# Optimization experiments

Measured on AMD Instinct MI355X. Metric: run time of the kernel, lower is better.

## Reference

```python
import jax, jax.numpy as jnp
import numpy as np

N_NODES, E_TOT, E_ACT = 20000, 250000, 200000
LAT, OH = 128, 128
M0, M1, M2 = 64, 32, 16            # irreps_out: 64x0e + 32x1o + 16x2e
D_IR = M0 + 3 * M1 + 5 * M2        # 240
G = M1 + M2                        # gate scalars (48)
T0 = M0 + G                        # tp m=0 scalar channels (112)
I0, I1, I2 = 3 * M0, 3 * M1, 3 * M2  # tp input muls (center|edge|neighbor)


def _split(x, m0, m1, m2):
    e = x.shape[0]
    return (x[:, :m0],
            x[:, m0:m0 + 3 * m1].reshape(e, m1, 3),
            x[:, m0 + 3 * m1:].reshape(e, m2, 5))


def _merge(s0, s1, s2):
    e = s0.shape[0]
    return jnp.concatenate([s0, s1.reshape(e, -1), s2.reshape(e, -1)], axis=-1)


def _mlp(x, ws, bs):
    for i, (w, b) in enumerate(zip(ws, bs)):
        x = x @ w + b
        if i < len(ws) - 1:
            x = jax.nn.silu(x)
    return x


def _forward(latents, node_features, edge_features, cutoff_coeffs, edge_one_hot,
             wigner_D1, wigner_D2,
             W0, W1r, W1i, W2r, W2i, Gw, Gb,
             P0, P0b, P1, P2, Ew, Eb, ln_g, ln_b,
             A1, A1b, A2, A2b, A3, A3b,
             B1, B1b, B2, B2b, B3, B3b,
             O0, O1, O2,
             edge_index, active_edges):
    ec = edge_index[0][active_edges]
    en = edge_index[1][active_edges]
    # gather node features per edge (equivariant_norm_type='none' -> identity norms)
    nc0, nc1, nc2 = _split(node_features[ec], M0, M1, M2)
    ef0, ef1, ef2 = _split(edge_features, M0, M1, M2)
    nn0, nn1, nn2 = _split(node_features[en], M0, M1, M2)
    x0 = jnp.concatenate([nc0, ef0, nn0], -1)   # [E,192]
    x1 = jnp.concatenate([nc1, ef1, nn1], 1)    # [E,96,3]
    x2 = jnp.concatenate([nc2, ef2, nn2], 1)    # [E,48,5]
    lat_a = latents[active_edges]
    # --- SO(2) linear: rotate into edge frame, per-m mixing, latent gains, rotate back ---
    r1 = jnp.einsum('eij,euj->eui', wigner_D1, x1)
    r2 = jnp.einsum('eij,euj->eui', wigner_D2, x2)
    in0 = jnp.concatenate([x0, r1[:, :, 1], r2[:, :, 2]], -1)   # m=0 [E,336]
    o_m0 = in0 @ W0.T                                           # [E,160]
    ip1 = jnp.concatenate([r1[:, :, 2], r2[:, :, 3]], -1)       # m=+1 [E,144]
    im1 = jnp.concatenate([r1[:, :, 0], r2[:, :, 1]], -1)       # m=-1
    op1 = ip1 @ W1r.T - im1 @ W1i.T                             # [E,48]
    on1 = ip1 @ W1i.T + im1 @ W1r.T
    op2 = r2[:, :, 4] @ W2r.T - r2[:, :, 0] @ W2i.T             # [E,16]
    on2 = r2[:, :, 4] @ W2i.T + r2[:, :, 0] @ W2r.T
    g = lat_a @ Gw + Gb                                         # per-edge gains [E,224]
    o_m0 = o_m0 * g[:, :160]
    g1 = g[:, 160:208]; g2 = g[:, 208:224]
    op1 = op1 * g1; on1 = on1 * g1; op2 = op2 * g2; on2 = on2 * g2
    y0 = o_m0[:, :T0]
    y1 = jnp.stack([on1[:, :M1], o_m0[:, T0:T0 + M1], op1[:, :M1]], -1)          # [E,32,3]
    y2 = jnp.stack([on2, on1[:, M1:], o_m0[:, T0 + M1:], op1[:, M1:], op2], -1)  # [E,16,5]
    y1 = jnp.einsum('eji,euj->eui', wigner_D1, y1)
    y2 = jnp.einsum('eji,euj->eui', wigner_D2, y2)
    # --- gate activation ---
    gates = jax.nn.sigmoid(y0[:, M0:])
    z0 = jax.nn.silu(y0[:, :M0])
    z1 = y1 * gates[:, :M1, None]
    z2 = y2 * gates[:, M1:, None]
    # --- lin_post: per-l channel mixing, fan-in normalized, bias on scalars ---
    z0 = z0 @ P0.T / np.sqrt(M0) + P0b
    z1 = jnp.einsum('uv,evm->eum', P1, z1) / np.sqrt(M1)
    z2 = jnp.einsum('uv,evm->eum', P2, z2) / np.sqrt(M2)
    scalars = z0                                               # taken before weighting
    # --- E3ElementLinear: per-edge per-channel weights from latents ---
    w = lat_a @ Ew + Eb                                        # [E,112]
    z0 = z0 * w[:, :M0]
    z1 = z1 * w[:, M0:M0 + M1, None]
    z2 = z2 * w[:, M0 + M1:, None]
    new_edge = _merge(z0, z1, z2)
    # --- latent update: LN -> mlp1(ln_lat||scalars) -> mlp2(h||one_hot) -> cutoff ---
    mu = lat_a.mean(-1, keepdims=True)
    var = ((lat_a - mu) ** 2).mean(-1, keepdims=True)
    ln_lat = (lat_a - mu) * jax.lax.rsqrt(var + 1e-5) * ln_g + ln_b
    h = _mlp(jnp.concatenate([ln_lat, scalars], -1), (A1, A2, A3), (A1b, A2b, A3b))
    h = _mlp(jnp.concatenate([h, edge_one_hot], -1), (B1, B2, B3), (B1b, B2b, B3b))
    new_lat = cutoff_coeffs[active_edges][:, None] * h
    # --- residual update (res_update_params buffer = 0) ---
    u = jax.nn.sigmoid(jnp.asarray(0.0, new_edge.dtype))
    c_old = jax.lax.rsqrt(u * u + 1.0)
    c_new = u * c_old
    edge_out = c_old * edge_features + c_new * new_edge        # identity residual path
    latents_out = latents.at[active_edges].set(c_new * new_lat + c_old * lat_a)
    # --- layer one-hot tensor product (uvu with 128x0e) ---
    f0, f1, f2 = _split(edge_out, M0, M1, M2)
    s = 1.0 / np.sqrt(OH)
    t0 = f0 * (edge_one_hot @ O0.T) * s
    t1 = f1 * (edge_one_hot @ O1.T)[:, :, None] * s
    t2 = f2 * (edge_one_hot @ O2.T)[:, :, None] * s
    edge_out = edge_out + _merge(t0, t1, t2)
    return edge_out, latents_out


def setup_inputs() -> dict:
    key = jax.random.key(0)
    ks = iter(jax.random.split(key, 64))
    nrm = lambda sh, s=0.05: jax.random.normal(next(ks), sh, jnp.float32) * s
    inp = dict(
        latents=nrm((E_TOT, LAT), 1.0),
        node_features=nrm((N_NODES, D_IR), 1.0),
        edge_features=nrm((E_ACT, D_IR), 1.0),
        cutoff_coeffs=jax.random.uniform(next(ks), (E_TOT,), jnp.float32),
        edge_one_hot=jax.random.uniform(next(ks), (E_ACT, OH), jnp.float32),
        wigner_D1=nrm((E_ACT, 3, 3), 0.5),
        wigner_D2=nrm((E_ACT, 5, 5), 0.3),
        W0=nrm((160, I0 + I1 + I2)), W1r=nrm((48, 144)), W1i=nrm((48, 144)),
        W2r=nrm((16, 48)), W2i=nrm((16, 48)),
        Gw=nrm((LAT, 224)), Gb=jnp.ones((224,), jnp.float32),
        P0=nrm((M0, M0)), P0b=nrm((M0,)), P1=nrm((M1, M1)), P2=nrm((M2, M2)),
        Ew=nrm((LAT, M0 + M1 + M2)), Eb=jnp.ones((M0 + M1 + M2,), jnp.float32),
        ln_g=jnp.ones((LAT,), jnp.float32), ln_b=jnp.zeros((LAT,), jnp.float32),
        A1=nrm((LAT + M0, LAT)), A1b=nrm((LAT,)),
        A2=nrm((LAT, LAT)), A2b=nrm((LAT,)),
        A3=nrm((LAT, LAT)), A3b=nrm((LAT,)),
        B1=nrm((LAT + OH, LAT)), B1b=nrm((LAT,)),
        B2=nrm((LAT, LAT)), B2b=nrm((LAT,)),
        B3=nrm((LAT, LAT)), B3b=nrm((LAT,)),
        O0=nrm((M0, OH)), O1=nrm((M1, OH)), O2=nrm((M2, OH)),
        edge_index=jax.random.randint(next(ks), (2, E_TOT), 0, N_NODES, jnp.int32),
        active_edges=jnp.sort(jax.random.permutation(next(ks), E_TOT)[:E_ACT]).astype(jnp.int32),
    )
    return inp


def reference(latents, node_features, edge_features, cutoff_coeffs, edge_one_hot,
              wigner_D1, wigner_D2,
              W0, W1r, W1i, W2r, W2i, Gw, Gb,
              P0, P0b, P1, P2, Ew, Eb, ln_g, ln_b,
              A1, A1b, A2, A2b, A3, A3b,
              B1, B1b, B2, B2b, B3, B3b,
              O0, O1, O2, edge_index, active_edges):
    return _forward(latents, node_features, edge_features, cutoff_coeffs, edge_one_hot,
                    wigner_D1, wigner_D2,
                    W0, W1r, W1i, W2r, W2i, Gw, Gb,
                    P0, P0b, P1, P2, Ew, Eb, ln_g, ln_b,
                    A1, A1b, A2, A2b, A3, A3b,
                    B1, B1b, B2, B2b, B3, B3b,
                    O0, O1, O2, edge_index, active_edges)
```

## Files before the change

### kernel.cpp

```cpp
#include <hip/hip_runtime.h>

typedef unsigned short us_t;
typedef short bf16x8 __attribute__((ext_vector_type(8)));
typedef float f32x4 __attribute__((ext_vector_type(4)));

#define E_ACT 200000
#define E_TOT 250000
#define DIR   240
#define C_OLD 0.8944271909999159f
#define C_NEW 0.4472135954999579f
#define S_OH  0.08838834764831845f

#define WO_W0   0
#define WO_W1P  56320
#define WO_W1M  70144
#define WO_W2P  83968
#define WO_W2M  85504
#define WO_GW   87040
#define WO_EW   115712
#define WO_A1   130048
#define WO_A2   154624
#define WO_A3   171008
#define WO_B1   187392
#define WO_B2   220160
#define WO_B3   236544
#define WO_O0   252928
#define WO_O1   261120
#define WO_O2   265216
#define WO_P0T  267264
#define WO_P1T  271360
#define WO_P2T  272384
#define W_TOTAL 272896

__device__ __forceinline__ float b2f(us_t u) { return __uint_as_float(((unsigned)u) << 16); }
__device__ __forceinline__ us_t f2b(float f) {
    unsigned x = __float_as_uint(f);
    return (us_t)((x + 0x7fffu + ((x >> 16) & 1u)) >> 16);
}
__device__ __forceinline__ float sigm(float x) { return 1.0f / (1.0f + __expf(-x)); }

#define MFMA(a,b,c) __builtin_amdgcn_mfma_f32_16x16x32_bf16((a),(b),(c),0,0,0)

__global__ __launch_bounds__(256) void prep_kernel(
    const float* __restrict__ W0, const float* __restrict__ W1r, const float* __restrict__ W1i,
    const float* __restrict__ W2r, const float* __restrict__ W2i,
    const float* __restrict__ Gw, const float* __restrict__ Ew,
    const float* __restrict__ A1, const float* __restrict__ A2, const float* __restrict__ A3,
    const float* __restrict__ B1, const float* __restrict__ B2, const float* __restrict__ B3,
    const float* __restrict__ O0, const float* __restrict__ O1, const float* __restrict__ O2,
    const float* __restrict__ P0w, const float* __restrict__ P1w, const float* __restrict__ P2w,
    us_t* __restrict__ wb)
{
    int idx = blockIdx.x * 256 + threadIdx.x;
    if (idx >= W_TOTAL) return;
    float v;
    if (idx < WO_W1P) {
        int r = idx, n = r / 352, k = r % 352;
        v = (k < 336) ? W0[n * 336 + k] : 0.f;
    } else if (idx < WO_W1M) {
        int r = idx - WO_W1P, n = r / 288, k = r % 288;
        v = (k < 144) ? W1r[n * 144 + k] : -W1i[n * 144 + (k - 144)];
    } else if (idx < WO_W2P) {
        int r = idx - WO_W1M, n = r / 288, k = r % 288;
        v = (k < 144) ? W1i[n * 144 + k] : W1r[n * 144 + (k - 144)];
    } else if (idx < WO_W2M) {
        int r = idx - WO_W2P, n = r / 96, k = r % 96;
        v = (k < 48) ? W2r[n * 48 + k] : -W2i[n * 48 + (k - 48)];
    } else if (idx < WO_GW) {
        int r = idx - WO_W2M, n = r / 96, k = r % 96;
        v = (k < 48) ? W2i[n * 48 + k] : W2r[n * 48 + (k - 48)];
    } else if (idx < WO_EW) {
        int r = idx - WO_GW, n = r / 128, k = r % 128;
        v = Gw[k * 224 + n];
    } else if (idx < WO_A1) {
        int r = idx - WO_EW, n = r / 128, k = r % 128;
        v = Ew[k * 112 + n];
    } else if (idx < WO_A2) {
        int r = idx - WO_A1, n = r / 192, k = r % 192;
        v = A1[k * 128 + n];
    } else if (idx < WO_A3) {
        int r = idx - WO_A2, n = r / 128, k = r % 128;
        v = A2[k * 128 + n];
    } else if (idx < WO_B1) {
        int r = idx - WO_A3, n = r / 128, k = r % 128;
        v = A3[k * 128 + n];
    } else if (idx < WO_B2) {
        int r = idx - WO_B1, n = r / 256, k = r % 256;
        v = B1[k * 128 + n];
    } else if (idx < WO_B3) {
        int r = idx - WO_B2, n = r / 128, k = r % 128;
        v = B2[k * 128 + n];
    } else if (idx < WO_O0) {
        int r = idx - WO_B3, n = r / 128, k = r % 128;
        v = B3[k * 128 + n];
    } else if (idx < WO_O1) {
        v = O0[idx - WO_O0];
    } else if (idx < WO_O2) {
        v = O1[idx - WO_O1];
    } else if (idx < WO_P0T) {
        v = O2[idx - WO_O2];
    } else if (idx < WO_P1T) {
        v = P0w[idx - WO_P0T];
    } else if (idx < WO_P2T) {
        v = P1w[idx - WO_P1T];
    } else {
        int r = idx - WO_P2T, n = r / 32, k = r % 32;
        v = (k < 16) ? P2w[n * 16 + k] : 0.f;
    }
    wb[idx] = f2b(v);
}

__device__ __forceinline__ void lat_fetch_a(const float* __restrict__ latents,
                                            const int* __restrict__ aes_l,
                                            int lane, bf16x8 a[4])
{
    const int r = lane & 15, g = lane >> 4;
    const float* lp = latents + (size_t)aes_l[r] * 128 + g * 8;
    #pragma unroll
    for (int ks = 0; ks < 4; ++ks) {
        float4 v0 = *(const float4*)(lp + ks * 32);
        float4 v1 = *(const float4*)(lp + ks * 32 + 4);
        bf16x8 av;
        av[0] = (short)f2b(v0.x); av[1] = (short)f2b(v0.y);
        av[2] = (short)f2b(v0.z); av[3] = (short)f2b(v0.w);
        av[4] = (short)f2b(v1.x); av[5] = (short)f2b(v1.y);
        av[6] = (short)f2b(v1.z); av[7] = (short)f2b(v1.w);
        a[ks] = av;
    }
}

__device__ __forceinline__ void gemmW0g(
    const us_t* __restrict__ in0s, const us_t* __restrict__ wbase,
    const bf16x8 latA[4], const float* __restrict__ Gb,
    int nt0, int nt1, us_t* __restrict__ om0g, int lane)
{
    const int r = lane & 15, g = lane >> 4;
    f32x4 w0a = {0.f,0.f,0.f,0.f}, w0b = w0a, ga = w0a, gb2 = w0a;
    const us_t* ap  = in0s + r * 360 + g * 8;
    const us_t* wp0 = wbase + WO_W0 + (size_t)(nt0 * 16 + r) * 352 + g * 8;
    const us_t* wp1 = wbase + WO_W0 + (size_t)(nt1 * 16 + r) * 352 + g * 8;
    #pragma unroll
    for (int ks = 0; ks < 11; ++ks) {
        bf16x8 a = *(const bf16x8*)(ap + ks * 32);
        w0a = MFMA(a, *(const bf16x8*)(wp0 + ks * 32), w0a);
        w0b = MFMA(a, *(const bf16x8*)(wp1 + ks * 32), w0b);
    }
    const us_t* gp0 = wbase + WO_GW + (size_t)(nt0 * 16 + r) * 128 + g * 8;
    const us_t* gp1 = wbase + WO_GW + (size_t)(nt1 * 16 + r) * 128 + g * 8;
    #pragma unroll
    for (int ks = 0; ks < 4; ++ks) {
        ga  = MFMA(latA[ks], *(const bf16x8*)(gp0 + ks * 32), ga);
        gb2 = MFMA(latA[ks], *(const bf16x8*)(gp1 + ks * 32), gb2);
    }
    float b0 = Gb[nt0 * 16 + r], b1 = Gb[nt1 * 16 + r];
    #pragma unroll
    for (int i = 0; i < 4; ++i) {
        int e = g * 4 + i;
        om0g[e * 162 + nt0 * 16 + r] = f2b(w0a[i] * (ga[i] + b0));
        om0g[e * 162 + nt1 * 16 + r] = f2b(w0b[i] * (gb2[i] + b1));
    }
}

__device__ __forceinline__ void gemmW1g(
    const us_t* __restrict__ cact1, const us_t* __restrict__ wbase,
    const bf16x8 latA[4], const float* __restrict__ Gb,
    int j, us_t* __restrict__ cp1g, us_t* __restrict__ cn1g, int lane)
{
    const int r = lane & 15, g = lane >> 4;
    f32x4 p = {0.f,0.f,0.f,0.f}, m = p, gg = p;
    const us_t* ap  = cact1 + r * 296 + g * 8;
    const us_t* wpP = wbase + WO_W1P + (size_t)(j * 16 + r) * 288 + g * 8;
    const us_t* wpM = wbase + WO_W1M + (size_t)(j * 16 + r) * 288 + g * 8;
    #pragma unroll
    for (int ks = 0; ks < 9; ++ks) {
        bf16x8 a = *(const bf16x8*)(ap + ks * 32);
        p = MFMA(a, *(const bf16x8*)(wpP + ks * 32), p);
        m = MFMA(a, *(const bf16x8*)(wpM + ks * 32), m);
    }
    const us_t* gp = wbase + WO_GW + (size_t)(160 + j * 16 + r) * 128 + g * 8;
    #pragma unroll
    for (int ks = 0; ks < 4; ++ks)
        gg = MFMA(latA[ks], *(const bf16x8*)(gp + ks * 32), gg);
    float gb = Gb[160 + j * 16 + r];
    #pragma unroll
    for (int i = 0; i < 4; ++i) {
        int e = g * 4 + i;
        float gv = gg[i] + gb;
        cp1g[e * 50 + j * 16 + r] = f2b(p[i] * gv);
        cn1g[e * 50 + j * 16 + r] = f2b(m[i] * gv);
    }
}

__device__ __forceinline__ void gemmW2g(
    const us_t* __restrict__ cact2, const us_t* __restrict__ wbase,
    const bf16x8 latA[4], const float* __restrict__ Gb,
    us_t* __restrict__ cp2g, us_t* __restrict__ cn2g, int lane)
{
    const int r = lane & 15, g = lane >> 4;
    f32x4 p = {0.f,0.f,0.f,0.f}, m = p, gg = p;
    const us_t* ap  = cact2 + r * 104 + g * 8;
    const us_t* wpP = wbase + WO_W2P + (size_t)r * 96 + g * 8;
    const us_t* wpM = wbase + WO_W2M + (size_t)r * 96 + g * 8;
    #pragma unroll
    for (int ks = 0; ks < 3; ++ks) {
        bf16x8 a = *(const bf16x8*)(ap + ks * 32);
        p = MFMA(a, *(const bf16x8*)(wpP + ks * 32), p);
        m = MFMA(a, *(const bf16x8*)(wpM + ks * 32), m);
    }
    const us_t* gp = wbase + WO_GW + (size_t)(208 + r) * 128 + g * 8;
    #pragma unroll
    for (int ks = 0; ks < 4; ++ks)
        gg = MFMA(latA[ks], *(const bf16x8*)(gp + ks * 32), gg);
    float gb = Gb[208 + r];
    #pragma unroll
    for (int i = 0; i < 4; ++i) {
        int e = g * 4 + i;
        float gv = gg[i] + gb;
        cp2g[e * 18 + r] = f2b(p[i] * gv);
        cn2g[e * 18 + r] = f2b(m[i] * gv);
    }
}

__device__ __forceinline__ void lat_gemm2(const bf16x8 a[4],
    const us_t* __restrict__ wgt, const float* __restrict__ bias,
    int nt0, int nt1, us_t* __restrict__ out, int os, int lane)
{
    const int r = lane & 15, g = lane >> 4;
    f32x4 acc0 = {0.f,0.f,0.f,0.f}, acc1 = {0.f,0.f,0.f,0.f};
    const us_t* wp0 = wgt + (size_t)(nt0 * 16 + r) * 128 + g * 8;
    const us_t* wp1 = wgt + (size_t)(nt1 * 16 + r) * 128 + g * 8;
    #pragma unroll
    for (int ks = 0; ks < 4; ++ks) {
        acc0 = MFMA(a[ks], *(const bf16x8*)(wp0 + ks * 32), acc0);
        acc1 = MFMA(a[ks], *(const bf16x8*)(wp1 + ks * 32), acc1);
    }
    float bi0 = bias[nt0 * 16 + r], bi1 = bias[nt1 * 16 + r];
    #pragma unroll
    for (int i = 0; i < 4; ++i) {
        int e = g * 4 + i;
        out[e * os + nt0 * 16 + r] = f2b(acc0[i] + bi0);
        out[e * os + nt1 * 16 + r] = f2b(acc1[i] + bi1);
    }
}

__device__ __forceinline__ void lat_gemm1(const bf16x8 a[4],
    const us_t* __restrict__ wgt, const float* __restrict__ bias,
    int nt, us_t* __restrict__ out, int os, int lane)
{
    const int r = lane & 15, g = lane >> 4;
    f32x4 acc = {0.f,0.f,0.f,0.f};
    const us_t* wp = wgt + (size_t)(nt * 16 + r) * 128 + g * 8;
    #pragma unroll
    for (int ks = 0; ks < 4; ++ks)
        acc = MFMA(a[ks], *(const bf16x8*)(wp + ks * 32), acc);
    float bi = bias[nt * 16 + r];
    #pragma unroll
    for (int i = 0; i < 4; ++i) {
        int e = g * 4 + i;
        out[e * os + nt * 16 + r] = f2b(acc[i] + bi);
    }
}

template<int KS>
__device__ __forceinline__ f32x4 pgemm(const us_t* __restrict__ actbase, int as,
                                       const us_t* __restrict__ wgt, int kp, int lane)
{
    const int r = lane & 15, g = lane >> 4;
    f32x4 acc = {0.f,0.f,0.f,0.f};
    const us_t* ap = actbase + r * as + g * 8;
    const us_t* wp = wgt + (size_t)r * kp + g * 8;
    #pragma unroll
    for (int ks = 0; ks < KS; ++ks) {
        bf16x8 a = *(const bf16x8*)(ap + ks * 32);
        bf16x8 b = *(const bf16x8*)(wp + ks * 32);
        acc = MFMA(a, b, acc);
    }
    return acc;
}

__global__ __launch_bounds__(256, 3) void k1_kernel(
    const float* __restrict__ latents,
    const float* __restrict__ node_features,
    const float* __restrict__ edge_features,
    const float* __restrict__ wD1,
    const float* __restrict__ wD2,
    const float* __restrict__ Gb,  const float* __restrict__ Eb,
    const float* __restrict__ P0b,
    const int* __restrict__ edge_index, const int* __restrict__ active_edges,
    const us_t* __restrict__ wbase,
    us_t* __restrict__ ne_ws, us_t* __restrict__ scal_ws)
{
    __shared__ __align__(16) char smem[40320];
    us_t* in0s  = (us_t*)(smem);
    us_t* cact1 = (us_t*)(smem + 11520);
    us_t* cact2 = (us_t*)(smem + 20992);
    float* D1l  = (float*)(smem + 24320);
    float* D2l  = (float*)(smem + 25088);
    int*   aes  = (int*)(smem + 26880);
    us_t* om0g  = (us_t*)(smem + 26944);
    us_t* cp1g  = (us_t*)(smem + 32128);
    us_t* cn1g  = (us_t*)(smem + 33728);
    us_t* cp2g  = (us_t*)(smem + 35328);
    us_t* cn2g  = (us_t*)(smem + 35904);
    us_t* wl    = (us_t*)(smem + 36480);
    us_t* z0l   = (us_t*)(smem);
    us_t* z1l   = (us_t*)(smem + 2304);
    us_t* z2l   = (us_t*)(smem + 5632);

    const int t  = threadIdx.x;
    const int e0 = blockIdx.x * 16;

    {
        const int e = t >> 4, l = t & 15;
        const int eg = e0 + e;
        const int ae = active_edges[eg];
        const int ec = edge_index[ae];
        const int en = edge_index[E_TOT + ae];
        if (l == 0) aes[e] = ae;

        float v1  = (l < 9) ? wD1[(size_t)eg * 9 + l] : 0.f;
        float v2a = wD2[(size_t)eg * 25 + l];
        float v2b = (l < 9) ? wD2[(size_t)eg * 25 + 16 + l] : 0.f;
        if (l < 9) D1l[e * 12 + l] = v1;
        D2l[e * 28 + l] = v2a;
        if (l < 9) D2l[e * 28 + 16 + l] = v2b;

        float d1[9], d2[25];
        #pragma unroll
        for (int i = 0; i < 9; ++i)  d1[i] = __shfl(v1, i, 16);
        #pragma unroll
        for (int i = 0; i < 16; ++i) d2[i] = __shfl(v2a, i, 16);
        #pragma unroll
        for (int i = 0; i < 9; ++i)  d2[16 + i] = __shfl(v2b, i, 16);

        const float* pc = node_features + (size_t)ec * DIR;
        const float* pe = edge_features + (size_t)eg * DIR;
        const float* pn = node_features + (size_t)en * DIR;
        us_t* in0 = in0s + e * 360;
        us_t* c1  = cact1 + e * 296;
        us_t* c2  = cact2 + e * 104;

        #pragma unroll
        for (int j = 0; j < 4; ++j) {
            int i = l + 16 * j;
            in0[i]       = f2b(pc[i]);
            in0[64 + i]  = f2b(pe[i]);
            in0[128 + i] = f2b(pn[i]);
        }
        in0[336 + l] = 0;

        #pragma unroll
        for (int jj = 0; jj < 6; ++jj) {
            int u = l + 16 * jj;
            int uu = u & 31;
            const float* sp = (u < 32 ? pc : (u < 64 ? pe : pn)) + 64 + uu * 3;
            float x0 = sp[0], x1 = sp[1], x2 = sp[2];
            float r0 = d1[0] * x0 + d1[1] * x1 + d1[2] * x2;
            float r1 = d1[3] * x0 + d1[4] * x1 + d1[5] * x2;
            float r2 = d1[6] * x0 + d1[7] * x1 + d1[8] * x2;
            c1[144 + u]  = f2b(r0);
            in0[192 + u] = f2b(r1);
            c1[u]        = f2b(r2);
        }
        #pragma unroll
        for (int jj = 0; jj < 3; ++jj) {
            int u = l + 16 * jj;
            int uu = u & 15;
            const float* sp = (u < 16 ? pc : (u < 32 ? pe : pn)) + 160 + uu * 5;
            float x0 = sp[0], x1 = sp[1], x2 = sp[2], x3 = sp[3], x4 = sp[4];
            float r[5];
            #pragma unroll
            for (int i = 0; i < 5; ++i)
                r[i] = d2[i * 5 + 0] * x0 + d2[i * 5 + 1] * x1 + d2[i * 5 + 2] * x2
                     + d2[i * 5 + 3] * x3 + d2[i * 5 + 4] * x4;
            c2[48 + u]   = f2b(r[0]);
            c1[240 + u]  = f2b(r[1]);
            in0[288 + u] = f2b(r[2]);
            c1[96 + u]   = f2b(r[3]);
            c2[u]        = f2b(r[4]);
        }
    }
    __syncthreads();

    {
        const int lane = t & 63, w = t >> 6;
        bf16x8 a[4];
        lat_fetch_a(latents, aes, lane, a);
        if (w == 0) {
            gemmW0g(in0s, wbase, a, Gb, 0, 1, om0g, lane);
            gemmW0g(in0s, wbase, a, Gb, 2, 3, om0g, lane);
        } else if (w == 1) {
            gemmW0g(in0s, wbase, a, Gb, 4, 5, om0g, lane);
            gemmW0g(in0s, wbase, a, Gb, 6, 7, om0g, lane);
        } else if (w == 2) {
            gemmW1g(cact1, wbase, a, Gb, 0, cp1g, cn1g, lane);
            gemmW1g(cact1, wbase, a, Gb, 1, cp1g, cn1g, lane);
            gemmW1g(cact1, wbase, a, Gb, 2, cp1g, cn1g, lane);
        } else {
            gemmW0g(in0s, wbase, a, Gb, 8, 9, om0g, lane);
            gemmW2g(cact2, wbase, a, Gb, cp2g, cn2g, lane);
            lat_gemm2(a, wbase + WO_EW, Eb, 0, 1, wl, 120, lane);
            lat_gemm2(a, wbase + WO_EW, Eb, 2, 3, wl, 120, lane);
            lat_gemm2(a, wbase + WO_EW, Eb, 4, 5, wl, 120, lane);
            lat_gemm1(a, wbase + WO_EW, Eb, 6, wl, 120, lane);
        }
    }
    __syncthreads();

    {
        const int e = t >> 4, l = t & 15;
        const float* D1e = D1l + e * 12;
        const float* D2e = D2l + e * 28;
        #pragma unroll
        for (int uu = 0; uu < 2; ++uu) {
            int u = l + uu * 16;
            float j0 = b2f(cn1g[e * 50 + u]);
            float j1 = b2f(om0g[e * 162 + 112 + u]);
            float j2 = b2f(cp1g[e * 50 + u]);
            float gate = sigm(b2f(om0g[e * 162 + 64 + u]));
            #pragma unroll
            for (int i = 0; i < 3; ++i) {
                float yr = D1e[0 * 3 + i] * j0 + D1e[1 * 3 + i] * j1 + D1e[2 * 3 + i] * j2;
                z1l[e * 104 + i * 32 + u] = f2b(yr * gate);
            }
        }
        {
            int u = l;
            float j0 = b2f(cn2g[e * 18 + u]);
            float j1 = b2f(cn1g[e * 50 + 32 + u]);
            float j2 = b2f(om0g[e * 162 + 144 + u]);
            float j3 = b2f(cp1g[e * 50 + 32 + u]);
            float j4 = b2f(cp2g[e * 18 + u]);
            float gate = sigm(b2f(om0g[e * 162 + 96 + u]));
            #pragma unroll
            for (int i = 0; i < 5; ++i) {
                float yr = D2e[0 * 5 + i] * j0 + D2e[1 * 5 + i] * j1 + D2e[2 * 5 + i] * j2
                         + D2e[3 * 5 + i] * j3 + D2e[4 * 5 + i] * j4;
                z2l[e * 168 + i * 32 + u] = f2b(yr * gate);
                z2l[e * 168 + i * 32 + 16 + u] = 0;
            }
        }
        #pragma unroll
        for (int ii = 0; ii < 4; ++ii) {
            int c = l + 16 * ii;
            float v = b2f(om0g[e * 162 + c]);
            z0l[e * 72 + c] = f2b(v * sigm(v));
        }
    }
    __syncthreads();

    {
        const int lane = t & 63, w = t >> 6;
        const int r = lane & 15, g = lane >> 4;
        if (w < 2) {
            #pragma unroll
            for (int jj = 0; jj < 2; ++jj) {
                int nt = 2 * w + jj;
                f32x4 acc = pgemm<2>(z0l, 72, wbase + WO_P0T + nt * 16 * 64, 64, lane);
                int n = nt * 16 + r;
                float bi = P0b[n];
                #pragma unroll
                for (int i = 0; i < 4; ++i) {
                    int e = g * 4 + i, eg = e0 + e;
                    float z0p = acc[i] * 0.125f + bi;
                    scal_ws[(size_t)eg * 64 + n] = f2b(z0p);
                    ne_ws[(size_t)eg * 240 + n] = f2b(z0p * b2f(wl[e * 120 + n]));
                }
            }
        } else if (w == 2) {
            #pragma unroll
            for (int m = 0; m < 3; ++m) {
                #pragma unroll
                for (int nt = 0; nt < 2; ++nt) {
                    f32x4 acc = pgemm<1>(z1l + m * 32, 104,
                                         wbase + WO_P1T + nt * 16 * 32, 32, lane);
                    int u = nt * 16 + r;
                    #pragma unroll
                    for (int i = 0; i < 4; ++i) {
                        int e = g * 4 + i, eg = e0 + e;
                        float wv = b2f(wl[e * 120 + 64 + u]);
                        ne_ws[(size_t)eg * 240 + 64 + u * 3 + m] =
                            f2b(acc[i] * 0.17677669529663687f * wv);
                    }
                }
            }
        } else if (w == 3) {
            #pragma unroll
            for (int m = 0; m < 5; ++m) {
                f32x4 acc = pgemm<1>(z2l + m * 32, 168, wbase + WO_P2T, 32, lane);
                int u = r;
                #pragma unroll
                for (int i = 0; i < 4; ++i) {
                    int e = g * 4 + i, eg = e0 + e;
                    float wv = b2f(wl[e * 120 + 96 + u]);
                    ne_ws[(size_t)eg * 240 + 160 + u * 5 + m] =
                        f2b(acc[i] * 0.25f * wv);
                }
            }
        }
    }
}

template<int KS, bool SILU>
__device__ __forceinline__ void mlayer(
    const us_t* __restrict__ actA, const us_t* __restrict__ actB, int split, int as,
    const us_t* __restrict__ wgt, int kp, const float* __restrict__ bias,
    us_t* __restrict__ out, int os, int lane, int w)
{
    const int r = lane & 15, g = lane >> 4;
    const int n0 = 2 * w * 16, n1 = n0 + 16;
    f32x4 a00 = {0.f,0.f,0.f,0.f}, a01 = a00, a10 = a00, a11 = a00;
    const us_t* wp0 = wgt + (size_t)(n0 + r) * kp + g * 8;
    const us_t* wp1 = wgt + (size_t)(n1 + r) * kp + g * 8;
    #pragma unroll
    for (int ks = 0; ks < KS; ++ks) {
        const us_t* ab = (ks < split) ? (actA + ks * 32) : (actB + (ks - split) * 32);
        bf16x8 f0 = *(const bf16x8*)(ab + r * as + g * 8);
        bf16x8 f1 = *(const bf16x8*)(ab + (16 + r) * as + g * 8);
        bf16x8 b0 = *(const bf16x8*)(wp0 + ks * 32);
        bf16x8 b1 = *(const bf16x8*)(wp1 + ks * 32);
        a00 = MFMA(f0, b0, a00); a01 = MFMA(f0, b1, a01);
        a10 = MFMA(f1, b0, a10); a11 = MFMA(f1, b1, a11);
    }
    float bi0 = bias[n0 + r], bi1 = bias[n1 + r];
    #pragma unroll
    for (int i = 0; i < 4; ++i) {
        int eA = g * 4 + i, eB = 16 + g * 4 + i;
        float v;
        v = a00[i] + bi0; if (SILU) v *= sigm(v); out[eA * os + n0 + r] = f2b(v);
        v = a01[i] + bi1; if (SILU) v *= sigm(v); out[eA * os + n1 + r] = f2b(v);
        v = a10[i] + bi0; if (SILU) v *= sigm(v); out[eB * os + n0 + r] = f2b(v);
        v = a11[i] + bi1; if (SILU) v *= sigm(v); out[eB * os + n1 + r] = f2b(v);
    }
}

__global__ __launch_bounds__(256) void k2_kernel(
    const float* __restrict__ latents, const float* __restrict__ cutoff,
    const float* __restrict__ one_hot,
    const float* __restrict__ ln_g, const float* __restrict__ ln_b,
    const float* __restrict__ A1b, const float* __restrict__ A2b, const float* __restrict__ A3b,
    const float* __restrict__ B1b, const float* __restrict__ B2b, const float* __restrict__ B3b,
    const int* __restrict__ active_edges,
    const us_t* __restrict__ wbase,
    const us_t* __restrict__ scal_ws, us_t* __restrict__ ohw_ws,
    float* __restrict__ out_lat)
{
    __shared__ __align__(16) char smem[39424];
    us_t* x_lds = (us_t*)(smem);
    us_t* h_a   = (us_t*)(smem + 12800);
    us_t* h_b   = (us_t*)(smem + 21504);
    us_t* ohl   = (us_t*)(smem + 30208);
    int*  aes_l = (int*)(smem + 38912);
    float* cut_l= (float*)(smem + 39040);

    const int t  = threadIdx.x;
    const int e0 = blockIdx.x * 32;
    const int lane = t & 63, w = t >> 6;

    {
        int ee = t >> 3, l8 = t & 7;
        int ae = active_edges[e0 + ee];
        if (l8 == 0) { aes_l[ee] = ae; cut_l[ee] = cutoff[ae]; }
        const float* lp = latents + (size_t)ae * 128 + l8 * 16;
        float xs[16];
        #pragma unroll
        for (int q = 0; q < 4; ++q) {
            float4 v = *(const float4*)(lp + q * 4);
            xs[q * 4 + 0] = v.x; xs[q * 4 + 1] = v.y;
            xs[q * 4 + 2] = v.z; xs[q * 4 + 3] = v.w;
        }
        float s1 = 0.f, s2 = 0.f;
        #pragma unroll
        for (int i = 0; i < 16; ++i) { s1 += xs[i]; s2 += xs[i] * xs[i]; }
        #pragma unroll
        for (int off = 1; off < 8; off <<= 1) {
            s1 += __shfl_xor(s1, off, 8);
            s2 += __shfl_xor(s2, off, 8);
        }
        float mu  = s1 * (1.f / 128.f);
        float var = s2 * (1.f / 128.f) - mu * mu;
        float rstd = rsqrtf(var + 1e-5f);
        #pragma unroll
        for (int i = 0; i < 16; ++i) {
            int li = l8 * 16 + i;
            x_lds[ee * 200 + li] = f2b((xs[i] - mu) * rstd * ln_g[li] + ln_b[li]);
        }
    }
    for (int idx = t; idx < 32 * 16; idx += 256) {
        int ee = idx >> 4, j = idx & 15;
        *(ushort4*)&x_lds[ee * 200 + 128 + j * 4] =
            *(const ushort4*)&scal_ws[(size_t)(e0 + ee) * 64 + j * 4];
    }
    for (int idx = t; idx < 32 * 32; idx += 256) {
        int ee = idx >> 5, j = idx & 31;
        float4 ov = *(const float4*)&one_hot[(size_t)(e0 + ee) * 128 + j * 4];
        ushort4 s; s.x = f2b(ov.x); s.y = f2b(ov.y); s.z = f2b(ov.z); s.w = f2b(ov.w);
        *(ushort4*)&ohl[ee * 136 + j * 4] = s;
    }
    __syncthreads();

    mlayer<6, true>(x_lds, x_lds, 6, 200, wbase + WO_A1, 192, A1b, h_a, 136, lane, w);
    __syncthreads();
    mlayer<4, true>(h_a, h_a, 4, 136, wbase + WO_A2, 128, A2b, h_b, 136, lane, w);
    __syncthreads();
    mlayer<4, false>(h_b, h_b, 4, 136, wbase + WO_A3, 128, A3b, h_a, 136, lane, w);
    __syncthreads();
    mlayer<8, true>(h_a, ohl, 4, 136, wbase + WO_B1, 256, B1b, h_b, 136, lane, w);
    __syncthreads();
    mlayer<4, true>(h_b, h_b, 4, 136, wbase + WO_B2, 128, B2b, h_a, 136, lane, w);
    __syncthreads();
    {
        const int r = lane & 15, g = lane >> 4;
        const int n0 = 2 * w * 16, n1 = n0 + 16;
        f32x4 a00 = {0.f,0.f,0.f,0.f}, a01 = a00, a10 = a00, a11 = a00;
        const us_t* wp0 = wbase + WO_B3 + (size_t)(n0 + r) * 128 + g * 8;
        const us_t* wp1 = wbase + WO_B3 + (size_t)(n1 + r) * 128 + g * 8;
        #pragma unroll
        for (int ks = 0; ks < 4; ++ks) {
            bf16x8 f0 = *(const bf16x8*)(h_a + ks * 32 + r * 136 + g * 8);
            bf16x8 f1 = *(const bf16x8*)(h_a + ks * 32 + (16 + r) * 136 + g * 8);
            bf16x8 b0 = *(const bf16x8*)(wp0 + ks * 32);
            bf16x8 b1 = *(const bf16x8*)(wp1 + ks * 32);
            a00 = MFMA(f0, b0, a00); a01 = MFMA(f0, b1, a01);
            a10 = MFMA(f1, b0, a10); a11 = MFMA(f1, b1, a11);
        }
        float bi0 = B3b[n0 + r], bi1 = B3b[n1 + r];
        #pragma unroll
        for (int i = 0; i < 4; ++i) {
            int eA = g * 4 + i, eB = 16 + g * 4 + i;
            int aeA = aes_l[eA], aeB = aes_l[eB];
            float cA = C_NEW * cut_l[eA], cB = C_NEW * cut_l[eB];
            float* oA = out_lat + (size_t)aeA * 128;
            float* oB = out_lat + (size_t)aeB * 128;
            const float* lA = latents + (size_t)aeA * 128;
            const float* lB = latents + (size_t)aeB * 128;
            oA[n0 + r] = cA * (a00[i] + bi0) + C_OLD * lA[n0 + r];
            oA[n1 + r] = cA * (a01[i] + bi1) + C_OLD * lA[n1 + r];
            oB[n0 + r] = cB * (a10[i] + bi0) + C_OLD * lB[n0 + r];
            oB[n1 + r] = cB * (a11[i] + bi1) + C_OLD * lB[n1 + r];
        }
    }

    {
        const int r = lane & 15, g = lane >> 4;
        const int cnt = (w == 3) ? 1 : 2;
        #pragma unroll
        for (int ii = 0; ii < 2; ++ii) {
            if (ii >= cnt) break;
            int nt = (ii == 0) ? w : w + 4;
            const us_t* wb2 = (nt < 4) ? (wbase + WO_O0 + (size_t)nt * 16 * 128)
                            : (nt < 6) ? (wbase + WO_O1 + (size_t)(nt - 4) * 16 * 128)
                                       : (wbase + WO_O2);
            f32x4 c0 = {0.f,0.f,0.f,0.f}, c1 = c0;
            const us_t* wp = wb2 + (size_t)r * 128 + g * 8;
            #pragma unroll
            for (int ks = 0; ks < 4; ++ks) {
                bf16x8 f0 = *(const bf16x8*)(ohl + ks * 32 + r * 136 + g * 8);
                bf16x8 f1 = *(const bf16x8*)(ohl + ks * 32 + (16 + r) * 136 + g * 8);
                bf16x8 b = *(const bf16x8*)(wp + ks * 32);
                c0 = MFMA(f0, b, c0); c1 = MFMA(f1, b, c1);
            }
            int n = nt * 16 + r;
            #pragma unroll
            for (int i = 0; i < 4; ++i) {
                int eA = e0 + g * 4 + i, eB = e0 + 16 + g * 4 + i;
                ohw_ws[(size_t)eA * 112 + n] = f2b(c0[i]);
                ohw_ws[(size_t)eB * 112 + n] = f2b(c1[i]);
            }
        }
    }
}

__global__ __launch_bounds__(256) void kfin_kernel(
    const float* __restrict__ edge_features, const us_t* __restrict__ ne_ws,
    const us_t* __restrict__ ohw_ws, float* __restrict__ out_edge)
{
    int idx = blockIdx.x * 256 + threadIdx.x;
    if (idx >= E_ACT * 60) return;
    int e = idx / 60;
    int c0 = (idx - e * 60) * 4;
    float4 ef = *(const float4*)&edge_features[(size_t)e * 240 + c0];
    ushort4 nv = *(const ushort4*)&ne_ws[(size_t)e * 240 + c0];
    float nef[4] = {b2f(nv.x), b2f(nv.y), b2f(nv.z), b2f(nv.w)};
    float eff[4] = {ef.x, ef.y, ef.z, ef.w};
    float4 ov;
    float* op = &ov.x;
    #pragma unroll
    for (int j = 0; j < 4; ++j) {
        int c = c0 + j;
        int o;
        if (c < 64)       o = c;
        else if (c < 160) o = 64 + (c - 64) / 3;
        else              o = 96 + (c - 160) / 5;
        float ohv = b2f(ohw_ws[(size_t)e * 112 + o]);
        op[j] = (C_OLD * eff[j] + C_NEW * nef[j]) * (1.f + S_OH * ohv);
    }
    *(float4*)&out_edge[(size_t)e * 240 + c0] = ov;
}

extern "C" void kernel_launch(void* const* d_in, const int* in_sizes, int n_in,
                              void* d_out, int out_size, void* d_ws, size_t ws_size,
                              hipStream_t stream)
{
    const float* latents  = (const float*)d_in[0];
    const float* node_f   = (const float*)d_in[1];
    const float* edge_f   = (const float*)d_in[2];
    const float* cutoff   = (const float*)d_in[3];
    const float* one_hot  = (const float*)d_in[4];
    const float* wD1      = (const float*)d_in[5];
    const float* wD2      = (const float*)d_in[6];
    const float* W0       = (const float*)d_in[7];
    const float* W1r      = (const float*)d_in[8];
    const float* W1i      = (const float*)d_in[9];
    const float* W2r      = (const float*)d_in[10];
    const float* W2i      = (const float*)d_in[11];
    const float* Gw       = (const float*)d_in[12];
    const float* Gb       = (const float*)d_in[13];
    const float* P0w      = (const float*)d_in[14];
    const float* P0b      = (const float*)d_in[15];
    const float* P1w      = (const float*)d_in[16];
    const float* P2w      = (const float*)d_in[17];
    const float* Ew       = (const float*)d_in[18];
    const float* Eb       = (const float*)d_in[19];
    const float* ln_g     = (const float*)d_in[20];
    const float* ln_b     = (const float*)d_in[21];
    const float* A1       = (const float*)d_in[22];
    const float* A1b      = (const float*)d_in[23];
    const float* A2       = (const float*)d_in[24];
    const float* A2b      = (const float*)d_in[25];
    const float* A3       = (const float*)d_in[26];
    const float* A3b      = (const float*)d_in[27];
    const float* B1       = (const float*)d_in[28];
    const float* B1b      = (const float*)d_in[29];
    const float* B2       = (const float*)d_in[30];
    const float* B2b      = (const float*)d_in[31];
    const float* B3       = (const float*)d_in[32];
    const float* B3b      = (const float*)d_in[33];
    const float* O0       = (const float*)d_in[34];
    const float* O1       = (const float*)d_in[35];
    const float* O2       = (const float*)d_in[36];
    const int* edge_index = (const int*)d_in[37];
    const int* act_e      = (const int*)d_in[38];

    float* out_edge = (float*)d_out;
    float* out_lat  = out_edge + (size_t)E_ACT * DIR;

    us_t* ne_ws   = (us_t*)d_ws;
    us_t* ohw_ws  = ne_ws + (size_t)E_ACT * DIR;
    us_t* scal_ws = ohw_ws + (size_t)E_ACT * 112;
    us_t* wbase   = scal_ws + (size_t)E_ACT * 64;

    prep_kernel<<<dim3((W_TOTAL + 255) / 256), dim3(256), 0, stream>>>(
        W0, W1r, W1i, W2r, W2i, Gw, Ew, A1, A2, A3, B1, B2, B3,
        O0, O1, O2, P0w, P1w, P2w, wbase);

    hipMemcpyAsync(out_lat, latents, (size_t)E_TOT * 128 * sizeof(float),
                   hipMemcpyDeviceToDevice, stream);

    k1_kernel<<<dim3(E_ACT / 16), dim3(256), 0, stream>>>(
        latents, node_f, edge_f, wD1, wD2, Gb, Eb, P0b,
        edge_index, act_e, wbase, ne_ws, scal_ws);

    k2_kernel<<<dim3(E_ACT / 32), dim3(256), 0, stream>>>(
        latents, cutoff, one_hot, ln_g, ln_b,
        A1b, A2b, A3b, B1b, B2b, B3b,
        act_e, wbase, scal_ws, ohw_ws, out_lat);

    kfin_kernel<<<dim3((E_ACT * 60 + 255) / 256), dim3(256), 0, stream>>>(
        edge_f, ne_ws, ohw_ws, out_edge);
}
```

Measured before the change: 806.6 us.

## Process 32 edges per block in k1 to reuse weight fragments across two M-tiles

k1 now handles 32 edges per block instead of 16. Each weight B-fragment loaded from global memory feeds two MFMAs, one per 16-edge half, which halves weight traffic per edge. The GEMM tiles are rebalanced across the four waves, LDS use roughly doubles to about 80 KB, and occupancy hints change to 2 blocks per CU for k1 and 3 for k2. In exchange, fewer blocks fit per CU, register pressure rises, and latency hiding may be weaker.

```diff
diff --git a/kernel.cpp b/kernel.cpp
--- a/kernel.cpp
+++ b/kernel.cpp
@@ -129,156 +129,157 @@
     }
 }
 
-__device__ __forceinline__ void gemmW0g(
+__device__ __forceinline__ void gemmW0g32(
     const us_t* __restrict__ in0s, const us_t* __restrict__ wbase,
-    const bf16x8 latA[4], const float* __restrict__ Gb,
-    int nt0, int nt1, us_t* __restrict__ om0g, int lane)
+    const bf16x8 lA[4], const bf16x8 lB[4], const float* __restrict__ Gb,
+    int nt, us_t* __restrict__ om0g, int lane)
 {
     const int r = lane & 15, g = lane >> 4;
-    f32x4 w0a = {0.f,0.f,0.f,0.f}, w0b = w0a, ga = w0a, gb2 = w0a;
-    const us_t* ap  = in0s + r * 360 + g * 8;
-    const us_t* wp0 = wbase + WO_W0 + (size_t)(nt0 * 16 + r) * 352 + g * 8;
-    const us_t* wp1 = wbase + WO_W0 + (size_t)(nt1 * 16 + r) * 352 + g * 8;
+    f32x4 wa = {0.f,0.f,0.f,0.f}, wb = wa, ga = wa, gb = wa;
+    const us_t* apA = in0s + r * 360 + g * 8;
+    const us_t* apB = in0s + (16 + r) * 360 + g * 8;
+    const us_t* wp  = wbase + WO_W0 + (size_t)(nt * 16 + r) * 352 + g * 8;
     #pragma unroll
     for (int ks = 0; ks < 11; ++ks) {
-        bf16x8 a = *(const bf16x8*)(ap + ks * 32);
-        w0a = MFMA(a, *(const bf16x8*)(wp0 + ks * 32), w0a);
-        w0b = MFMA(a, *(const bf16x8*)(wp1 + ks * 32), w0b);
-    }
-    const us_t* gp0 = wbase + WO_GW + (size_t)(nt0 * 16 + r) * 128 + g * 8;
-    const us_t* gp1 = wbase + WO_GW + (size_t)(nt1 * 16 + r) * 128 + g * 8;
+        bf16x8 b = *(const bf16x8*)(wp + ks * 32);
+        wa = MFMA(*(const bf16x8*)(apA + ks * 32), b, wa);
+        wb = MFMA(*(const bf16x8*)(apB + ks * 32), b, wb);
+    }
+    const us_t* gp = wbase + WO_GW + (size_t)(nt * 16 + r) * 128 + g * 8;
     #pragma unroll
     for (int ks = 0; ks < 4; ++ks) {
-        ga  = MFMA(latA[ks], *(const bf16x8*)(gp0 + ks * 32), ga);
-        gb2 = MFMA(latA[ks], *(const bf16x8*)(gp1 + ks * 32), gb2);
-    }
-    float b0 = Gb[nt0 * 16 + r], b1 = Gb[nt1 * 16 + r];
+        bf16x8 b = *(const bf16x8*)(gp + ks * 32);
+        ga = MFMA(lA[ks], b, ga);
+        gb = MFMA(lB[ks], b, gb);
+    }
+    float bi = Gb[nt * 16 + r];
     #pragma unroll
     for (int i = 0; i < 4; ++i) {
-        int e = g * 4 + i;
-        om0g[e * 162 + nt0 * 16 + r] = f2b(w0a[i] * (ga[i] + b0));
-        om0g[e * 162 + nt1 * 16 + r] = f2b(w0b[i] * (gb2[i] + b1));
-    }
-}
-
-__device__ __forceinline__ void gemmW1g(
+        int eA = g * 4 + i, eB = 16 + g * 4 + i;
+        om0g[eA * 162 + nt * 16 + r] = f2b(wa[i] * (ga[i] + bi));
+        om0g[eB * 162 + nt * 16 + r] = f2b(wb[i] * (gb[i] + bi));
+    }
+}
+
+__device__ __forceinline__ void gemmW1g32(
     const us_t* __restrict__ cact1, const us_t* __restrict__ wbase,
-    const bf16x8 latA[4], const float* __restrict__ Gb,
+    const bf16x8 lA[4], const bf16x8 lB[4], const float* __restrict__ Gb,
     int j, us_t* __restrict__ cp1g, us_t* __restrict__ cn1g, int lane)
 {
     const int r = lane & 15, g = lane >> 4;
-    f32x4 p = {0.f,0.f,0.f,0.f}, m = p, gg = p;
-    const us_t* ap  = cact1 + r * 296 + g * 8;
+    f32x4 pa = {0.f,0.f,0.f,0.f}, pb = pa, ma = pa, mb = pa, ga = pa, gb = pa;
+    const us_t* apA = cact1 + r * 296 + g * 8;
+    const us_t* apB = cact1 + (16 + r) * 296 + g * 8;
     const us_t* wpP = wbase + WO_W1P + (size_t)(j * 16 + r) * 288 + g * 8;
     const us_t* wpM = wbase + WO_W1M + (size_t)(j * 16 + r) * 288 + g * 8;
     #pragma unroll
     for (int ks = 0; ks < 9; ++ks) {
-        bf16x8 a = *(const bf16x8*)(ap + ks * 32);
-        p = MFMA(a, *(const bf16x8*)(wpP + ks * 32), p);
-        m = MFMA(a, *(const bf16x8*)(wpM + ks * 32), m);
+        bf16x8 aA = *(const bf16x8*)(apA + ks * 32);
+        bf16x8 aB = *(const bf16x8*)(apB + ks * 32);
+        bf16x8 bP = *(const bf16x8*)(wpP + ks * 32);
+        bf16x8 bM = *(const bf16x8*)(wpM + ks * 32);
+        pa = MFMA(aA, bP, pa); pb = MFMA(aB, bP, pb);
+        ma = MFMA(aA, bM, ma); mb = MFMA(aB, bM, mb);
     }
     const us_t* gp = wbase + WO_GW + (size_t)(160 + j * 16 + r) * 128 + g * 8;
     #pragma unroll
-    for (int ks = 0; ks < 4; ++ks)
-        gg = MFMA(latA[ks], *(const bf16x8*)(gp + ks * 32), gg);
-    float gb = Gb[160 + j * 16 + r];
+    for (int ks = 0; ks < 4; ++ks) {
+        bf16x8 b = *(const bf16x8*)(gp + ks * 32);
+        ga = MFMA(lA[ks], b, ga);
+        gb = MFMA(lB[ks], b, gb);
+    }
+    float bi = Gb[160 + j * 16 + r];
     #pragma unroll
     for (int i = 0; i < 4; ++i) {
-        int e = g * 4 + i;
-        float gv = gg[i] + gb;
-        cp1g[e * 50 + j * 16 + r] = f2b(p[i] * gv);
-        cn1g[e * 50 + j * 16 + r] = f2b(m[i] * gv);
-    }
-}
-
-__device__ __forceinline__ void gemmW2g(
+        int eA = g * 4 + i, eB = 16 + g * 4 + i;
+        float gA = ga[i] + bi, gB = gb[i] + bi;
+        cp1g[eA * 50 + j * 16 + r] = f2b(pa[i] * gA);
+        cn1g[eA * 50 + j * 16 + r] = f2b(ma[i] * gA);
+        cp1g[eB * 50 + j * 16 + r] = f2b(pb[i] * gB);
+        cn1g[eB * 50 + j * 16 + r] = f2b(mb[i] * gB);
+    }
+}
+
+__device__ __forceinline__ void gemmW2g32(
     const us_t* __restrict__ cact2, const us_t* __restrict__ wbase,
-    const bf16x8 latA[4], const float* __restrict__ Gb,
+    const bf16x8 lA[4], const bf16x8 lB[4], const float* __restrict__ Gb,
     us_t* __restrict__ cp2g, us_t* __restrict__ cn2g, int lane)
 {
     const int r = lane & 15, g = lane >> 4;
-    f32x4 p = {0.f,0.f,0.f,0.f}, m = p, gg = p;
-    const us_t* ap  = cact2 + r * 104 + g * 8;
+    f32x4 pa = {0.f,0.f,0.f,0.f}, pb = pa, ma = pa, mb = pa, ga = pa, gb = pa;
+    const us_t* apA = cact2 + r * 104 + g * 8;
+    const us_t* apB = cact2 + (16 + r) * 104 + g * 8;
     const us_t* wpP = wbase + WO_W2P + (size_t)r * 96 + g * 8;
     const us_t* wpM = wbase + WO_W2M + (size_t)r * 96 + g * 8;
     #pragma unroll
     for (int ks = 0; ks < 3; ++ks) {
-        bf16x8 a = *(const bf16x8*)(ap + ks * 32);
-        p = MFMA(a, *(const bf16x8*)(wpP + ks * 32), p);
-        m = MFMA(a, *(const bf16x8*)(wpM + ks * 32), m);
+        bf16x8 aA = *(const bf16x8*)(apA + ks * 32);
+        bf16x8 aB = *(const bf16x8*)(apB + ks * 32);
+        bf16x8 bP = *(const bf16x8*)(wpP + ks * 32);
+        bf16x8 bM = *(const bf16x8*)(wpM + ks * 32);
+        pa = MFMA(aA, bP, pa); pb = MFMA(aB, bP, pb);
+        ma = MFMA(aA, bM, ma); mb = MFMA(aB, bM, mb);
     }
     const us_t* gp = wbase + WO_GW + (size_t)(208 + r) * 128 + g * 8;
     #pragma unroll
-    for (int ks = 0; ks < 4; ++ks)
-        gg = MFMA(latA[ks], *(const bf16x8*)(gp + ks * 32), gg);
-    float gb = Gb[208 + r];
+    for (int ks = 0; ks < 4; ++ks) {
+        bf16x8 b = *(const bf16x8*)(gp + ks * 32);
+        ga = MFMA(lA[ks], b, ga);
+        gb = MFMA(lB[ks], b, gb);
+    }
+    float bi = Gb[208 + r];
     #pragma unroll
     for (int i = 0; i < 4; ++i) {
-        int e = g * 4 + i;
-        float gv = gg[i] + gb;
-        cp2g[e * 18 + r] = f2b(p[i] * gv);
-        cn2g[e * 18 + r] = f2b(m[i] * gv);
-    }
-}
-
-__device__ __forceinline__ void lat_gemm2(const bf16x8 a[4],
+        int eA = g * 4 + i, eB = 16 + g * 4 + i;
+        float gA = ga[i] + bi, gB = gb[i] + bi;
+        cp2g[eA * 18 + r] = f2b(pa[i] * gA);
+        cn2g[eA * 18 + r] = f2b(ma[i] * gA);
+        cp2g[eB * 18 + r] = f2b(pb[i] * gB);
+        cn2g[eB * 18 + r] = f2b(mb[i] * gB);
+    }
+}
+
+__device__ __forceinline__ void lat_gemmE32(
+    const bf16x8 lA[4], const bf16x8 lB[4],
     const us_t* __restrict__ wgt, const float* __restrict__ bias,
-    int nt0, int nt1, us_t* __restrict__ out, int os, int lane)
+    int nt, us_t* __restrict__ wl, int lane)
 {
     const int r = lane & 15, g = lane >> 4;
-    f32x4 acc0 = {0.f,0.f,0.f,0.f}, acc1 = {0.f,0.f,0.f,0.f};
-    const us_t* wp0 = wgt + (size_t)(nt0 * 16 + r) * 128 + g * 8;
-    const us_t* wp1 = wgt + (size_t)(nt1 * 16 + r) * 128 + g * 8;
+    f32x4 aA = {0.f,0.f,0.f,0.f}, aB = aA;
+    const us_t* wp = wgt + (size_t)(nt * 16 + r) * 128 + g * 8;
     #pragma unroll
     for (int ks = 0; ks < 4; ++ks) {
-        acc0 = MFMA(a[ks], *(const bf16x8*)(wp0 + ks * 32), acc0);
-        acc1 = MFMA(a[ks], *(const bf16x8*)(wp1 + ks * 32), acc1);
-    }
-    float bi0 = bias[nt0 * 16 + r], bi1 = bias[nt1 * 16 + r];
+        bf16x8 b = *(const bf16x8*)(wp + ks * 32);
+        aA = MFMA(lA[ks], b, aA);
+        aB = MFMA(lB[ks], b, aB);
+    }
+    float bi = bias[nt * 16 + r];
     #pragma unroll
     for (int i = 0; i < 4; ++i) {
-        int e = g * 4 + i;
-        out[e * os + nt0 * 16 + r] = f2b(acc0[i] + bi0);
-        out[e * os + nt1 * 16 + r] = f2b(acc1[i] + bi1);
-    }
-}
-
-__device__ __forceinline__ void lat_gemm1(const bf16x8 a[4],
-    const us_t* __restrict__ wgt, const float* __restrict__ bias,
-    int nt, us_t* __restrict__ out, int os, int lane)
+        int eA = g * 4 + i, eB = 16 + g * 4 + i;
+        wl[eA * 120 + nt * 16 + r] = f2b(aA[i] + bi);
+        wl[eB * 120 + nt * 16 + r] = f2b(aB[i] + bi);
+    }
+}
+
+template<int KS>
+__device__ __forceinline__ void pgemm32(const us_t* __restrict__ actbase, int as,
+                                        const us_t* __restrict__ wgt, int kp, int lane,
+                                        f32x4& accA, f32x4& accB)
 {
     const int r = lane & 15, g = lane >> 4;
-    f32x4 acc = {0.f,0.f,0.f,0.f};
-    const us_t* wp = wgt + (size_t)(nt * 16 + r) * 128 + g * 8;
-    #pragma unroll
-    for (int ks = 0; ks < 4; ++ks)
-        acc = MFMA(a[ks], *(const bf16x8*)(wp + ks * 32), acc);
-    float bi = bias[nt * 16 + r];
-    #pragma unroll
-    for (int i = 0; i < 4; ++i) {
-        int e = g * 4 + i;
-        out[e * os + nt * 16 + r] = f2b(acc[i] + bi);
-    }
-}
-
-template<int KS>
-__device__ __forceinline__ f32x4 pgemm(const us_t* __restrict__ actbase, int as,
-                                       const us_t* __restrict__ wgt, int kp, int lane)
-{
-    const int r = lane & 15, g = lane >> 4;
-    f32x4 acc = {0.f,0.f,0.f,0.f};
-    const us_t* ap = actbase + r * as + g * 8;
+    const us_t* apA = actbase + r * as + g * 8;
+    const us_t* apB = actbase + (16 + r) * as + g * 8;
     const us_t* wp = wgt + (size_t)r * kp + g * 8;
     #pragma unroll
     for (int ks = 0; ks < KS; ++ks) {
-        bf16x8 a = *(const bf16x8*)(ap + ks * 32);
         bf16x8 b = *(const bf16x8*)(wp + ks * 32);
-        acc = MFMA(a, b, acc);
-    }
-    return acc;
-}
-
-__global__ __launch_bounds__(256, 3) void k1_kernel(
+        accA = MFMA(*(const bf16x8*)(apA + ks * 32), b, accA);
+        accB = MFMA(*(const bf16x8*)(apB + ks * 32), b, accB);
+    }
+}
+
+__global__ __launch_bounds__(256, 2) void k1_kernel(
     const float* __restrict__ latents,
     const float* __restrict__ node_features,
     const float* __restrict__ edge_features,
@@ -290,28 +291,29 @@
     const us_t* __restrict__ wbase,
     us_t* __restrict__ ne_ws, us_t* __restrict__ scal_ws)
 {
-    __shared__ __align__(16) char smem[40320];
+    __shared__ __align__(16) char smem[80640];
     us_t* in0s  = (us_t*)(smem);
-    us_t* cact1 = (us_t*)(smem + 11520);
-    us_t* cact2 = (us_t*)(smem + 20992);
-    float* D1l  = (float*)(smem + 24320);
-    float* D2l  = (float*)(smem + 25088);
-    int*   aes  = (int*)(smem + 26880);
-    us_t* om0g  = (us_t*)(smem + 26944);
-    us_t* cp1g  = (us_t*)(smem + 32128);
-    us_t* cn1g  = (us_t*)(smem + 33728);
-    us_t* cp2g  = (us_t*)(smem + 35328);
-    us_t* cn2g  = (us_t*)(smem + 35904);
-    us_t* wl    = (us_t*)(smem + 36480);
+    us_t* cact1 = (us_t*)(smem + 23040);
+    us_t* cact2 = (us_t*)(smem + 41984);
+    float* D1l  = (float*)(smem + 48640);
+    float* D2l  = (float*)(smem + 50176);
+    int*   aes  = (int*)(smem + 53760);
+    us_t* om0g  = (us_t*)(smem + 53888);
+    us_t* cp1g  = (us_t*)(smem + 64256);
+    us_t* cn1g  = (us_t*)(smem + 67456);
+    us_t* cp2g  = (us_t*)(smem + 70656);
+    us_t* cn2g  = (us_t*)(smem + 71808);
+    us_t* wl    = (us_t*)(smem + 72960);
     us_t* z0l   = (us_t*)(smem);
-    us_t* z1l   = (us_t*)(smem + 2304);
-    us_t* z2l   = (us_t*)(smem + 5632);
+    us_t* z1l   = (us_t*)(smem + 4608);
+    us_t* z2l   = (us_t*)(smem + 11264);
 
     const int t  = threadIdx.x;
-    const int e0 = blockIdx.x * 16;
-
-    {
-        const int e = t >> 4, l = t & 15;
+    const int e0 = blockIdx.x * 32;
+
+    #pragma unroll
+    for (int ep = 0; ep < 2; ++ep) {
+        const int e = (t >> 4) + 16 * ep, l = t & 15;
         const int eg = e0 + e;
         const int ae = active_edges[eg];
         const int ec = edge_index[ae];
@@ -384,31 +386,37 @@
 
     {
         const int lane = t & 63, w = t >> 6;
-        bf16x8 a[4];
-        lat_fetch_a(latents, aes, lane, a);
+        bf16x8 lA[4], lB[4];
+        lat_fetch_a(latents, aes, lane, lA);
+        lat_fetch_a(latents, aes + 16, lane, lB);
         if (w == 0) {
-            gemmW0g(in0s, wbase, a, Gb, 0, 1, om0g, lane);
-            gemmW0g(in0s, wbase, a, Gb, 2, 3, om0g, lane);
+            gemmW0g32(in0s, wbase, lA, lB, Gb, 0, om0g, lane);
+            gemmW0g32(in0s, wbase, lA, lB, Gb, 1, om0g, lane);
+            gemmW0g32(in0s, wbase, lA, lB, Gb, 2, om0g, lane);
+            gemmW1g32(cact1, wbase, lA, lB, Gb, 0, cp1g, cn1g, lane);
         } else if (w == 1) {
-            gemmW0g(in0s, wbase, a, Gb, 4, 5, om0g, lane);
-            gemmW0g(in0s, wbase, a, Gb, 6, 7, om0g, lane);
+            gemmW0g32(in0s, wbase, lA, lB, Gb, 3, om0g, lane);
+            gemmW0g32(in0s, wbase, lA, lB, Gb, 4, om0g, lane);
+            gemmW0g32(in0s, wbase, lA, lB, Gb, 5, om0g, lane);
+            gemmW1g32(cact1, wbase, lA, lB, Gb, 1, cp1g, cn1g, lane);
         } else if (w == 2) {
-            gemmW1g(cact1, wbase, a, Gb, 0, cp1g, cn1g, lane);
-            gemmW1g(cact1, wbase, a, Gb, 1, cp1g, cn1g, lane);
-            gemmW1g(cact1, wbase, a, Gb, 2, cp1g, cn1g, lane);
+            gemmW0g32(in0s, wbase, lA, lB, Gb, 6, om0g, lane);
+            gemmW0g32(in0s, wbase, lA, lB, Gb, 7, om0g, lane);
+            gemmW0g32(in0s, wbase, lA, lB, Gb, 8, om0g, lane);
+            gemmW1g32(cact1, wbase, lA, lB, Gb, 2, cp1g, cn1g, lane);
         } else {
-            gemmW0g(in0s, wbase, a, Gb, 8, 9, om0g, lane);
-            gemmW2g(cact2, wbase, a, Gb, cp2g, cn2g, lane);
-            lat_gemm2(a, wbase + WO_EW, Eb, 0, 1, wl, 120, lane);
-            lat_gemm2(a, wbase + WO_EW, Eb, 2, 3, wl, 120, lane);
-            lat_gemm2(a, wbase + WO_EW, Eb, 4, 5, wl, 120, lane);
-            lat_gemm1(a, wbase + WO_EW, Eb, 6, wl, 120, lane);
-        }
-    }
-    __syncthreads();
-
-    {
-        const int e = t >> 4, l = t & 15;
+            gemmW0g32(in0s, wbase, lA, lB, Gb, 9, om0g, lane);
+            gemmW2g32(cact2, wbase, lA, lB, Gb, cp2g, cn2g, lane);
+            #pragma unroll
+            for (int nt = 0; nt < 7; ++nt)
+                lat_gemmE32(lA, lB, wbase + WO_EW, Eb, nt, wl, lane);
+        }
+    }
+    __syncthreads();
+
+    #pragma unroll
+    for (int ep = 0; ep < 2; ++ep) {
+        const int e = (t >> 4) + 16 * ep, l = t & 15;
         const float* D1e = D1l + e * 12;
         const float* D2e = D2l + e * 28;
         #pragma unroll
@@ -452,19 +460,24 @@
     {
         const int lane = t & 63, w = t >> 6;
         const int r = lane & 15, g = lane >> 4;
+        const float sc1 = 0.17677669529663687f;
         if (w < 2) {
             #pragma unroll
             for (int jj = 0; jj < 2; ++jj) {
                 int nt = 2 * w + jj;
-                f32x4 acc = pgemm<2>(z0l, 72, wbase + WO_P0T + nt * 16 * 64, 64, lane);
+                f32x4 aA = {0.f,0.f,0.f,0.f}, aB = aA;
+                pgemm32<2>(z0l, 72, wbase + WO_P0T + nt * 16 * 64, 64, lane, aA, aB);
                 int n = nt * 16 + r;
                 float bi = P0b[n];
                 #pragma unroll
                 for (int i = 0; i < 4; ++i) {
-                    int e = g * 4 + i, eg = e0 + e;
-                    float z0p = acc[i] * 0.125f + bi;
-                    scal_ws[(size_t)eg * 64 + n] = f2b(z0p);
-                    ne_ws[(size_t)eg * 240 + n] = f2b(z0p * b2f(wl[e * 120 + n]));
+                    int eA = g * 4 + i, eB = 16 + g * 4 + i;
+                    float zA = aA[i] * 0.125f + bi;
+                    float zB = aB[i] * 0.125f + bi;
+                    scal_ws[(size_t)(e0 + eA) * 64 + n] = f2b(zA);
+                    scal_ws[(size_t)(e0 + eB) * 64 + n] = f2b(zB);
+                    ne_ws[(size_t)(e0 + eA) * 240 + n] = f2b(zA * b2f(wl[eA * 120 + n]));
+                    ne_ws[(size_t)(e0 + eB) * 240 + n] = f2b(zB * b2f(wl[eB * 120 + n]));
                 }
             }
         } else if (w == 2) {
@@ -472,29 +485,33 @@
             for (int m = 0; m < 3; ++m) {
                 #pragma unroll
                 for (int nt = 0; nt < 2; ++nt) {
-                    f32x4 acc = pgemm<1>(z1l + m * 32, 104,
-                                         wbase + WO_P1T + nt * 16 * 32, 32, lane);
+                    f32x4 aA = {0.f,0.f,0.f,0.f}, aB = aA;
+                    pgemm32<1>(z1l + m * 32, 104, wbase + WO_P1T + nt * 16 * 32, 32,
+                               lane, aA, aB);
                     int u = nt * 16 + r;
                     #pragma unroll
                     for (int i = 0; i < 4; ++i) {
-                        int e = g * 4 + i, eg = e0 + e;
-                        float wv = b2f(wl[e * 120 + 64 + u]);
-                        ne_ws[(size_t)eg * 240 + 64 + u * 3 + m] =
-                            f2b(acc[i] * 0.17677669529663687f * wv);
+                        int eA = g * 4 + i, eB = 16 + g * 4 + i;
+                        ne_ws[(size_t)(e0 + eA) * 240 + 64 + u * 3 + m] =
+                            f2b(aA[i] * sc1 * b2f(wl[eA * 120 + 64 + u]));
+                        ne_ws[(size_t)(e0 + eB) * 240 + 64 + u * 3 + m] =
+                            f2b(aB[i] * sc1 * b2f(wl[eB * 120 + 64 + u]));
                     }
                 }
             }
         } else if (w == 3) {
             #pragma unroll
             for (int m = 0; m < 5; ++m) {
-                f32x4 acc = pgemm<1>(z2l + m * 32, 168, wbase + WO_P2T, 32, lane);
+                f32x4 aA = {0.f,0.f,0.f,0.f}, aB = aA;
+                pgemm32<1>(z2l + m * 32, 168, wbase + WO_P2T, 32, lane, aA, aB);
                 int u = r;
                 #pragma unroll
                 for (int i = 0; i < 4; ++i) {
-                    int e = g * 4 + i, eg = e0 + e;
-                    float wv = b2f(wl[e * 120 + 96 + u]);
-                    ne_ws[(size_t)eg * 240 + 160 + u * 5 + m] =
-                        f2b(acc[i] * 0.25f * wv);
+                    int eA = g * 4 + i, eB = 16 + g * 4 + i;
+                    ne_ws[(size_t)(e0 + eA) * 240 + 160 + u * 5 + m] =
+                        f2b(aA[i] * 0.25f * b2f(wl[eA * 120 + 96 + u]));
+                    ne_ws[(size_t)(e0 + eB) * 240 + 160 + u * 5 + m] =
+                        f2b(aB[i] * 0.25f * b2f(wl[eB * 120 + 96 + u]));
                 }
             }
         }
@@ -534,7 +551,7 @@
     }
 }
 
-__global__ __launch_bounds__(256) void k2_kernel(
+__global__ __launch_bounds__(256, 3) void k2_kernel(
     const float* __restrict__ latents, const float* __restrict__ cutoff,
     const float* __restrict__ one_hot,
     const float* __restrict__ ln_g, const float* __restrict__ ln_b,
@@ -757,7 +774,7 @@
     hipMemcpyAsync(out_lat, latents, (size_t)E_TOT * 128 * sizeof(float),
                    hipMemcpyDeviceToDevice, stream);
 
-    k1_kernel<<<dim3(E_ACT / 16), dim3(256), 0, stream>>>(
+    k1_kernel<<<dim3(E_ACT / 32), dim3(256), 0, stream>>>(
         latents, node_f, edge_f, wD1, wD2, Gb, Eb, P0b,
         edge_index, act_e, wbase, ne_ws, scal_ws);
 
```

New measurement: 713.6 us. -11.5%, faster.
